# Kernel optimization log

Hardware: AMD Instinct MI355X
Metric: run time of the kernel (lower is better)

The kernel has to match this reference:

```python
import jax, jax.numpy as jnp
import numpy as np

BN_EPS = 1e-5

def _square_distance(a, b):
    # a: (B,N,3), b: (B,M,3) -> (B,N,M) squared euclidean distance
    a2 = jnp.sum(a * a, axis=-1)[:, :, None]
    b2 = jnp.sum(b * b, axis=-1)[:, None, :]
    return a2 + b2 - 2.0 * jnp.einsum('bnd,bmd->bnm', a, b)

def _bn(x, gamma, beta, mean, var):
    # eval-mode batchnorm over channel (last) dim
    return (x - mean) * jax.lax.rsqrt(var + BN_EPS) * gamma + beta

def setup_inputs() -> dict:
    key = jax.random.key(0)
    ks = jax.random.split(key, 16)
    B, M, N, D, C = 4, 2048, 16384, 64, 64
    din, dout = C + D, 64
    return {
        'xyz_down': jax.random.normal(ks[0], (B, M, 3), jnp.float32),
        'xyz_up': jax.random.normal(ks[1], (B, N, 3), jnp.float32),
        'feat_down': jax.random.normal(ks[2], (B, M, D), jnp.float32),
        'feat_up': jax.random.normal(ks[3], (B, N, C), jnp.float32),
        'W1': jax.random.normal(ks[4], (din, din), jnp.float32) * 0.05,
        'b1': jax.random.normal(ks[5], (din,), jnp.float32) * 0.05,
        'bn1_gamma': jax.random.uniform(ks[6], (din,), jnp.float32, 0.5, 1.5),
        'bn1_beta': jax.random.normal(ks[7], (din,), jnp.float32) * 0.05,
        'bn1_mean': jax.random.normal(ks[8], (din,), jnp.float32) * 0.05,
        'bn1_var': jax.random.uniform(ks[9], (din,), jnp.float32, 0.5, 1.5),
        'W2': jax.random.normal(ks[10], (dout, din), jnp.float32) * 0.05,
        'b2': jax.random.normal(ks[11], (dout,), jnp.float32) * 0.05,
        'bn2_gamma': jax.random.uniform(ks[12], (dout,), jnp.float32, 0.5, 1.5),
        'bn2_beta': jax.random.normal(ks[13], (dout,), jnp.float32) * 0.05,
        'bn2_mean': jax.random.normal(ks[14], (dout,), jnp.float32) * 0.05,
        'bn2_var': jax.random.uniform(ks[15], (dout,), jnp.float32, 0.5, 1.5),
    }

def reference(xyz_down, xyz_up, feat_down, feat_up,
              W1, b1, bn1_gamma, bn1_beta, bn1_mean, bn1_var,
              W2, b2, bn2_gamma, bn2_beta, bn2_mean, bn2_var):
    dist = _square_distance(xyz_up, xyz_down)              # (B,N,M)
    dist_recip = 1.0 / (dist + 1e-8)
    weight = dist_recip / jnp.sum(dist_recip, axis=2, keepdims=True)
    # bmm-equivalent of the original broadcast-multiply-sum
    feat_interp = jnp.einsum('bnm,bmd->bnd', weight, feat_down)  # (B,N,D)
    x = jnp.concatenate([feat_up, feat_interp], axis=-1)   # (B,N,C+D)
    # Conv1d(k=1) == pointwise linear over channel dim
    x = jnp.einsum('bnc,oc->bno', x, W1) + b1
    x = jax.nn.relu(_bn(x, bn1_gamma, bn1_beta, bn1_mean, bn1_var))
    x = jnp.einsum('bnc,oc->bno', x, W2) + b2
    x = _bn(x, bn2_gamma, bn2_beta, bn2_mean, bn2_var)
    return x
```

## Files before the change

kernel.cpp:

```cpp
#include <hip/hip_runtime.h>

typedef unsigned short u16;
typedef unsigned int   u32;
typedef unsigned long long u64;

typedef __attribute__((ext_vector_type(8))) short bf16x8;
typedef __attribute__((ext_vector_type(4))) float f32x4;

#define BB 4
#define MM 2048
#define NN 16384
#define DD 64

__device__ __forceinline__ u16 f2bf(float f) {
    union { float f; u32 u; } v; v.f = f;
    u32 r = v.u + 0x7fffu + ((v.u >> 16) & 1u);
    return (u16)(r >> 16);
}

__device__ __forceinline__ u32 pack_trunc(float hi, float lo) {
    union { float f; u32 u; } a, b; a.f = hi; b.f = lo;
    return __builtin_amdgcn_perm(a.u, b.u, 0x07060302);
}

__device__ __forceinline__ u32 pack_rne(float hi, float lo) {
    return (u32)f2bf(lo) | ((u32)f2bf(hi) << 16);
}

__device__ __forceinline__ bf16x8 pack8(float4 p, float4 q) {
    bf16x8 v;
    v[0] = (short)f2bf(p.x); v[1] = (short)f2bf(p.y);
    v[2] = (short)f2bf(p.z); v[3] = (short)f2bf(p.w);
    v[4] = (short)f2bf(q.x); v[5] = (short)f2bf(q.y);
    v[6] = (short)f2bf(q.z); v[7] = (short)f2bf(q.w);
    return v;
}

#define OFF_INTERP 0ull
#define OFF_FDT    8388608ull
#define OFF_XYZ    9437184ull
#define OFF_W1     9568256ull
#define OFF_W2     9601024ull
#define OFF_BN     9617408ull
#define WS_NEED    9618944ull

__global__ __launch_bounds__(256)
void prep4_kernel(const float* __restrict__ xyz_down,
                  const float* __restrict__ feat_down,
                  const float* __restrict__ W1, const float* __restrict__ b1,
                  const float* __restrict__ g1, const float* __restrict__ be1,
                  const float* __restrict__ m1, const float* __restrict__ v1,
                  const float* __restrict__ W2, const float* __restrict__ b2,
                  const float* __restrict__ g2, const float* __restrict__ be2,
                  const float* __restrict__ m2, const float* __restrict__ v2,
                  u16* __restrict__ fdT, float4* __restrict__ xyzd2,
                  u16* __restrict__ w1bf, u16* __restrict__ w2bf,
                  float* __restrict__ bnbuf)
{
    const int blk = blockIdx.x, t = threadIdx.x;
    if (blk < 128) {
        __shared__ u16 T[64 * 70];
        const int b = blk >> 5, m0 = (blk & 31) * 64;
        {
            const int row = t >> 2, fcb = (t & 3) * 16;
            const float4* src = (const float4*)(feat_down + ((size_t)(b * MM + m0 + row)) * 64 + fcb);
#pragma unroll
            for (int i = 0; i < 4; i++) {
                float4 v = src[i];
                union { u16 h[4]; u64 q; } pk;
                pk.h[0] = f2bf(v.x); pk.h[1] = f2bf(v.y);
                pk.h[2] = f2bf(v.z); pk.h[3] = f2bf(v.w);
                *(u64*)&T[row * 70 + fcb + i * 4] = pk.q;
            }
        }
        __syncthreads();
        {
            const int d = t & 63, w = t >> 6;
            union { u16 h[16]; uint4 q[2]; } o;
#pragma unroll
            for (int j = 0; j < 16; j++) o.h[j] = T[(w * 16 + j) * 70 + d];
            uint4* dst = (uint4*)&fdT[((size_t)(b * 64 + d)) * MM + m0 + w * 16];
            dst[0] = o.q[0];
            dst[1] = o.q[1];
        }
    } else if (blk < 160) {
        int idx = (blk - 128) * 256 + t;
        float x = xyz_down[idx * 3 + 0], y = xyz_down[idx * 3 + 1], z = xyz_down[idx * 3 + 2];
        xyzd2[idx] = make_float4(-2.f * x, -2.f * y, -2.f * z,
                                 x * x + y * y + z * z + 1e-8f);
    } else if (blk < 168) {
        int g = (blk - 160) * 256 + t;
        const float4* s = (const float4*)(W1 + g * 8);
        bf16x8 v = pack8(s[0], s[1]);
        *(bf16x8*)&w1bf[g * 8] = v;
    } else if (blk < 172) {
        int g = (blk - 168) * 256 + t;
        const float4* s = (const float4*)(W2 + g * 8);
        bf16x8 v = pack8(s[0], s[1]);
        *(bf16x8*)&w2bf[g * 8] = v;
    } else {
        if (t < 128) {
            float a = g1[t] * rsqrtf(v1[t] + 1e-5f);
            bnbuf[t] = a;
            bnbuf[128 + t] = (b1[t] - m1[t]) * a + be1[t];
        } else if (t < 192) {
            int o = t - 128;
            float a = g2[o] * rsqrtf(v2[o] + 1e-5f);
            bnbuf[256 + o] = a;
            bnbuf[320 + o] = (b2[o] - m2[o]) * a + be2[o];
        }
    }
}

__global__ __launch_bounds__(256, 4)
void interp4_kernel(const float* __restrict__ xyz_up,
                    const u16* __restrict__ fdT,
                    const float4* __restrict__ xyzd2,
                    u16* __restrict__ interp_out)
{
    __shared__ u16    ftbuf[2][64 * 72];
    __shared__ float4 xyzb[2][72];

    const int tid = threadIdx.x;
    const int b  = blockIdx.x >> 8;
    const int n0 = (blockIdx.x & 255) * 64;
    const int wave = tid >> 6;
    const int lane = tid & 63;
    const int q    = lane >> 4;
    const int nl   = lane & 15;

    const int row = n0 + wave * 16 + nl;
    const float* xu = xyz_up + ((size_t)(b * NN + row)) * 3;
    const float ax = xu[0], ay = xu[1], az = xu[2];
    const float a2 = ax * ax + ay * ay + az * az;

    f32x4 acc[4];
#pragma unroll
    for (int i = 0; i < 4; i++) acc[i] = (f32x4){0.f, 0.f, 0.f, 0.f};
    f32x4 accd = (f32x4){0.f, 0.f, 0.f, 0.f};

    bf16x8 ones;
#pragma unroll
    for (int i = 0; i < 8; i++) ones[i] = (short)0x3F80;

    const int sd = tid >> 2, sms = (tid & 3) * 16;
    const u16* fsrc = fdT + ((size_t)(b * 64 + sd)) * MM + sms;
    const float4* xsrc = xyzd2 + b * MM;

    {
        u16* fd = &ftbuf[0][sd * 72 + sms];
        *(uint4*)fd       = *(const uint4*)(fsrc);
        *(uint4*)(fd + 8) = *(const uint4*)(fsrc + 8);
        if (tid < 64) xyzb[0][tid + (tid >> 3)] = xsrc[tid];
    }
    __syncthreads();

    for (int c = 0; c < 32; ++c) {
        const int cur = c & 1, nxt = cur ^ 1;
        const bool have_next = (c + 1) < 32;
        uint4 nf0, nf1; float4 nx;
        if (have_next) {
            const int mc = (c + 1) * 64;
            nf0 = *(const uint4*)(fsrc + mc);
            nf1 = *(const uint4*)(fsrc + mc + 8);
            if (tid < 64) nx = xsrc[mc + tid];
        }

#pragma unroll
        for (int kk = 0; kk < 2; kk++) {
            u32 fr[4];
#pragma unroll
            for (int jp = 0; jp < 4; jp++) {
                int m0 = kk * 32 + q * 8 + jp * 2;
                int s0 = m0 + (m0 >> 3);
                float4 p0 = xyzb[cur][s0];
                float4 p1 = xyzb[cur][s0 + 1];
                float d0 = fmaf(p0.x, ax, fmaf(p0.y, ay, fmaf(p0.z, az, p0.w + a2)));
                float d1 = fmaf(p1.x, ax, fmaf(p1.y, ay, fmaf(p1.z, az, p1.w + a2)));
                d0 = fmaxf(d0, 1e-8f);
                d1 = fmaxf(d1, 1e-8f);
                float r0 = __builtin_amdgcn_rcpf(d0);
                float r1 = __builtin_amdgcn_rcpf(d1);
                fr[jp] = pack_trunc(r1, r0);
            }
            union { u32 u[4]; bf16x8 v; } af;
            af.u[0] = fr[0]; af.u[1] = fr[1]; af.u[2] = fr[2]; af.u[3] = fr[3];
#pragma unroll
            for (int dt = 0; dt < 4; dt++) {
                bf16x8 bb = *(bf16x8*)&ftbuf[cur][(dt * 16 + nl) * 72 + kk * 32 + q * 8];
                acc[dt] = __builtin_amdgcn_mfma_f32_16x16x32_bf16(af.v, bb, acc[dt], 0, 0, 0);
            }
            accd = __builtin_amdgcn_mfma_f32_16x16x32_bf16(af.v, ones, accd, 0, 0, 0);
        }

        if (have_next) {
            u16* fd = &ftbuf[nxt][sd * 72 + sms];
            *(uint4*)fd       = nf0;
            *(uint4*)(fd + 8) = nf1;
            if (tid < 64) xyzb[nxt][tid + (tid >> 3)] = nx;
        }
        __syncthreads();
    }

#pragma unroll
    for (int reg = 0; reg < 4; reg++) {
        int r = wave * 16 + q * 4 + reg;
        float inv = 1.0f / accd[reg];
        size_t gbase = ((size_t)(b * NN + n0 + r)) * 64;
#pragma unroll
        for (int dt = 0; dt < 4; dt++)
            interp_out[gbase + dt * 16 + nl] = f2bf(acc[dt][reg] * inv);
    }
}

__global__ __launch_bounds__(256, 2)
void mlp4_kernel(const float* __restrict__ feat_up,
                 const u16* __restrict__ interp,
                 const u16* __restrict__ w1bf,
                 const u16* __restrict__ w2bf,
                 const float* __restrict__ bnbuf,
                 float* __restrict__ out)
{
    __shared__ u16   w1L[128 * 136];
    __shared__ u16   w2L[64 * 136];
    __shared__ u16   xh[64 * 136];
    __shared__ float bnl[384];

    const int tid = threadIdx.x;
    const int b    = blockIdx.x >> 7;
    const int base = (blockIdx.x & 127) * 128;
    const int wave = tid >> 6;
    const int lane = tid & 63;
    const int q    = lane >> 4;
    const int nl   = lane & 15;

    bnl[tid] = bnbuf[tid];
    if (tid < 128) bnl[256 + tid] = bnbuf[256 + tid];

    {
        const int o = tid >> 1, h = (tid & 1) * 64;
        const uint4* src = (const uint4*)(w1bf + (size_t)o * 128 + h);
        uint4* dst = (uint4*)&w1L[o * 136 + h];
#pragma unroll
        for (int i = 0; i < 8; i++) dst[i] = src[i];
    }
    {
        const int o = tid >> 2, h = (tid & 3) * 32;
        const uint4* src = (const uint4*)(w2bf + (size_t)o * 128 + h);
        uint4* dst = (uint4*)&w2L[o * 136 + h];
#pragma unroll
        for (int i = 0; i < 4; i++) dst[i] = src[i];
    }

    for (int tile = 0; tile < 2; tile++) {
        const int n0 = base + tile * 64;
        __syncthreads();

        {
            const int r = tid >> 2, seg = (tid & 3) * 16;
            const float4* fs = (const float4*)(feat_up + ((size_t)(b * NN + n0 + r)) * 64 + seg);
            uint4* xd = (uint4*)&xh[r * 136 + seg];
            float4 f0 = fs[0], f1 = fs[1], f2 = fs[2], f3 = fs[3];
            uint4 o0, o1;
            o0.x = pack_rne(f0.y, f0.x); o0.y = pack_rne(f0.w, f0.z);
            o0.z = pack_rne(f1.y, f1.x); o0.w = pack_rne(f1.w, f1.z);
            o1.x = pack_rne(f2.y, f2.x); o1.y = pack_rne(f2.w, f2.z);
            o1.z = pack_rne(f3.y, f3.x); o1.w = pack_rne(f3.w, f3.z);
            xd[0] = o0; xd[1] = o1;
            const uint4* is = (const uint4*)(interp + ((size_t)(b * NN + n0 + r)) * 64 + seg);
            uint4* xd2 = (uint4*)&xh[r * 136 + 64 + seg];
            xd2[0] = is[0]; xd2[1] = is[1];
        }
        __syncthreads();

        f32x4 acc1[8];
#pragma unroll
        for (int i = 0; i < 8; i++) acc1[i] = (f32x4){0.f, 0.f, 0.f, 0.f};
#pragma unroll
        for (int k0 = 0; k0 < 128; k0 += 32) {
            bf16x8 af = *(bf16x8*)&xh[(wave * 16 + nl) * 136 + k0 + q * 8];
#pragma unroll
            for (int ot = 0; ot < 8; ot++) {
                bf16x8 bf = *(bf16x8*)&w1L[(ot * 16 + nl) * 136 + k0 + q * 8];
                acc1[ot] = __builtin_amdgcn_mfma_f32_16x16x32_bf16(af, bf, acc1[ot], 0, 0, 0);
            }
        }
        __syncthreads();

#pragma unroll
        for (int ot = 0; ot < 8; ot++) {
            int o = ot * 16 + nl;
            float aa = bnl[o], bc = bnl[128 + o];
#pragma unroll
            for (int reg = 0; reg < 4; reg++) {
                float v = fmaxf(fmaf(acc1[ot][reg], aa, bc), 0.f);
                xh[(wave * 16 + q * 4 + reg) * 136 + o] = f2bf(v);
            }
        }
        __syncthreads();

        f32x4 acc2[4];
#pragma unroll
        for (int i = 0; i < 4; i++) acc2[i] = (f32x4){0.f, 0.f, 0.f, 0.f};
#pragma unroll
        for (int k0 = 0; k0 < 128; k0 += 32) {
            bf16x8 af = *(bf16x8*)&xh[(wave * 16 + nl) * 136 + k0 + q * 8];
#pragma unroll
            for (int ot = 0; ot < 4; ot++) {
                bf16x8 bf = *(bf16x8*)&w2L[(ot * 16 + nl) * 136 + k0 + q * 8];
                acc2[ot] = __builtin_amdgcn_mfma_f32_16x16x32_bf16(af, bf, acc2[ot], 0, 0, 0);
            }
        }
        float* of = (float*)xh;
#pragma unroll
        for (int ot = 0; ot < 4; ot++) {
            int o = ot * 16 + nl;
            float aa = bnl[256 + o], bc = bnl[320 + o];
#pragma unroll
            for (int reg = 0; reg < 4; reg++)
                of[(wave * 16 + q * 4 + reg) * 68 + o] = fmaf(acc2[ot][reg], aa, bc);
        }
        __syncthreads();

        {
            const int r = tid >> 2, seg = (tid & 3) * 16;
            const float4* sf = (const float4*)&of[r * 68 + seg];
            float4* dst = (float4*)(out + ((size_t)(b * NN + n0 + r)) * 64 + seg);
#pragma unroll
            for (int i = 0; i < 4; i++) dst[i] = sf[i];
        }
    }
}

#define TN 128
#define BM 64
#define RS 72
#define FS 72

__global__ __launch_bounds__(256, 3)
void interp_kernel(const float* __restrict__ xyz_down,
                   const float* __restrict__ xyz_up,
                   const float* __restrict__ feat_down,
                   u16* __restrict__ interp_out)
{
    __shared__ u16   rbuf[TN * RS];
    __shared__ u16   ftbuf[DD * FS];
    __shared__ float xyzb[BM * 3];
    __shared__ float denp[TN * 2];
    __shared__ float invden[TN];

    const int tid = threadIdx.x;
    const int b  = blockIdx.x >> 7;
    const int n0 = (blockIdx.x & 127) * TN;

    const int nl_r = tid >> 1;
    const int half = tid & 1;
    const float* xu = xyz_up + (size_t)(b * NN + n0 + nl_r) * 3;
    const float ax = xu[0], ay = xu[1], az = xu[2];

    denp[tid] = 0.f;

    const int wave = tid >> 6;
    const int lane = tid & 63;
    const int q    = lane >> 4;
    const int nl   = lane & 15;

    f32x4 acc[2][4];
#pragma unroll
    for (int i = 0; i < 2; i++)
#pragma unroll
        for (int j = 0; j < 4; j++) acc[i][j] = (f32x4){0.f, 0.f, 0.f, 0.f};

    const int sm = (tid & 31) * 2;
    const int sd = (tid >> 5) * 8;

    for (int mc = 0; mc < MM; mc += BM) {
        __syncthreads();
        if (tid < 192) xyzb[tid] = xyz_down[(size_t)(b * MM + mc) * 3 + tid];
        {
            const float4* f0 = (const float4*)(feat_down + (size_t)(b * MM + mc + sm) * DD + sd);
            const float4* f1 = (const float4*)(feat_down + (size_t)(b * MM + mc + sm + 1) * DD + sd);
            float4 a0 = f0[0], a1 = f0[1];
            float4 b0 = f1[0], b1 = f1[1];
            float r0[8] = {a0.x, a0.y, a0.z, a0.w, a1.x, a1.y, a1.z, a1.w};
            float r1[8] = {b0.x, b0.y, b0.z, b0.w, b1.x, b1.y, b1.z, b1.w};
#pragma unroll
            for (int j = 0; j < 8; j++) {
                u32 pk = (u32)f2bf(r0[j]) | ((u32)f2bf(r1[j]) << 16);
                *(u32*)&ftbuf[(sd + j) * FS + sm] = pk;
            }
        }
        __syncthreads();
        {
            float dlc = 0.f;
#pragma unroll
            for (int s = 0; s < 4; s++) {
                bf16x8 v;
#pragma unroll
                for (int j = 0; j < 8; j++) {
                    int m = half * 32 + s * 8 + j;
                    float dx = ax - xyzb[3 * m + 0];
                    float dy = ay - xyzb[3 * m + 1];
                    float dz = az - xyzb[3 * m + 2];
                    float d = fmaf(dx, dx, fmaf(dy, dy, dz * dz)) + 1e-8f;
                    float r = __builtin_amdgcn_rcpf(d);
                    dlc += r;
                    v[j] = (short)f2bf(r);
                }
                *(bf16x8*)&rbuf[nl_r * RS + half * 32 + s * 8] = v;
            }
            denp[nl_r * 2 + half] += dlc;
        }
        __syncthreads();
        {
            const int rowbase = wave * 32;
#pragma unroll
            for (int k0 = 0; k0 < BM; k0 += 32) {
                bf16x8 a0 = *(bf16x8*)&rbuf[(rowbase + nl) * RS + k0 + q * 8];
                bf16x8 a1 = *(bf16x8*)&rbuf[(rowbase + 16 + nl) * RS + k0 + q * 8];
#pragma unroll
                for (int dt = 0; dt < 4; dt++) {
                    bf16x8 bb = *(bf16x8*)&ftbuf[(dt * 16 + nl) * FS + k0 + q * 8];
                    acc[0][dt] = __builtin_amdgcn_mfma_f32_16x16x32_bf16(a0, bb, acc[0][dt], 0, 0, 0);
                    acc[1][dt] = __builtin_amdgcn_mfma_f32_16x16x32_bf16(a1, bb, acc[1][dt], 0, 0, 0);
                }
            }
        }
    }

    __syncthreads();
    if (tid < TN) invden[tid] = 1.0f / (denp[tid * 2] + denp[tid * 2 + 1]);
    __syncthreads();
    {
        const int rowbase = wave * 32;
#pragma unroll
        for (int nt = 0; nt < 2; nt++) {
#pragma unroll
            for (int reg = 0; reg < 4; reg++) {
                int nloc = rowbase + nt * 16 + q * 4 + reg;
                float inv = invden[nloc];
                size_t gbase = (size_t)(b * NN + n0 + nloc) * DD;
#pragma unroll
                for (int dt = 0; dt < 4; dt++)
                    interp_out[gbase + dt * 16 + nl] = f2bf(acc[nt][dt][reg] * inv);
            }
        }
    }
}

#define T2 64

__global__ __launch_bounds__(256, 1)
void mlp_kernel(const float* __restrict__ feat_up,
                const u16*   __restrict__ interp,
                const float* __restrict__ W1, const float* __restrict__ b1,
                const float* __restrict__ g1, const float* __restrict__ be1,
                const float* __restrict__ m1, const float* __restrict__ v1,
                const float* __restrict__ W2, const float* __restrict__ b2,
                const float* __restrict__ g2, const float* __restrict__ be2,
                const float* __restrict__ m2, const float* __restrict__ v2,
                float* __restrict__ out)
{
    __shared__ u16 xb[T2 * 136];
    __shared__ u16 hb[T2 * 136];
    __shared__ u16 w1b[128 * 136];
    __shared__ u16 w2b[64 * 136];
    __shared__ float A1[128], Bc1[128], A2[64], Bc2[64];

    const int tid = threadIdx.x;
    const int b  = blockIdx.x >> 8;
    const int n0 = (blockIdx.x & 255) * T2;
    const int wave = tid >> 6;
    const int lane = tid & 63;
    const int q    = lane >> 4;
    const int nl   = lane & 15;

    if (tid < 128) {
        float a = g1[tid] * rsqrtf(v1[tid] + 1e-5f);
        A1[tid]  = a;
        Bc1[tid] = (b1[tid] - m1[tid]) * a + be1[tid];
    } else if (tid < 192) {
        int o = tid - 128;
        float a = g2[o] * rsqrtf(v2[o] + 1e-5f);
        A2[o]  = a;
        Bc2[o] = (b2[o] - m2[o]) * a + be2[o];
    }
    {
        const float4* src = (const float4*)(W1 + (size_t)(tid >> 1) * 128 + (tid & 1) * 64);
        u16* dst = &w1b[(tid >> 1) * 136 + (tid & 1) * 64];
#pragma unroll
        for (int i = 0; i < 8; i++)
            *(bf16x8*)(dst + 8 * i) = pack8(src[2 * i], src[2 * i + 1]);
    }
    {
        const float4* src = (const float4*)(W2 + (size_t)(tid >> 2) * 128 + (tid & 3) * 32);
        u16* dst = &w2b[(tid >> 2) * 136 + (tid & 3) * 32];
#pragma unroll
        for (int i = 0; i < 4; i++)
            *(bf16x8*)(dst + 8 * i) = pack8(src[2 * i], src[2 * i + 1]);
    }
    if (tid < 128) {
        int n = tid >> 1, hf = tid & 1;
        const float4* src = (const float4*)(feat_up + (size_t)(b * NN + n0 + n) * 64 + hf * 32);
        u16* dst = &xb[n * 136 + hf * 32];
#pragma unroll
        for (int i = 0; i < 4; i++)
            *(bf16x8*)(dst + 8 * i) = pack8(src[2 * i], src[2 * i + 1]);
    } else {
        int t2 = tid - 128;
        int n = t2 >> 1, hf = t2 & 1;
        const uint4* src = (const uint4*)(interp + (size_t)(b * NN + n0 + n) * 64 + hf * 32);
        u16* dst = &xb[n * 136 + 64 + hf * 32];
#pragma unroll
        for (int i = 0; i < 4; i++)
            *(uint4*)(dst + 8 * i) = src[i];
    }
    __syncthreads();

    f32x4 acc1[8];
#pragma unroll
    for (int i = 0; i < 8; i++) acc1[i] = (f32x4){0.f, 0.f, 0.f, 0.f};
#pragma unroll
    for (int k0 = 0; k0 < 128; k0 += 32) {
        bf16x8 a = *(bf16x8*)&xb[(wave * 16 + nl) * 136 + k0 + q * 8];
#pragma unroll
        for (int ot = 0; ot < 8; ot++) {
            bf16x8 bb = *(bf16x8*)&w1b[(ot * 16 + nl) * 136 + k0 + q * 8];
            acc1[ot] = __builtin_amdgcn_mfma_f32_16x16x32_bf16(a, bb, acc1[ot], 0, 0, 0);
        }
    }
#pragma unroll
    for (int ot = 0; ot < 8; ot++) {
        int o = ot * 16 + nl;
        float aa = A1[o], bc = Bc1[o];
#pragma unroll
        for (int reg = 0; reg < 4; reg++) {
            float v = fmaxf(fmaf(acc1[ot][reg], aa, bc), 0.f);
            hb[(wave * 16 + q * 4 + reg) * 136 + o] = f2bf(v);
        }
    }
    __syncthreads();

    f32x4 acc2[4];
#pragma unroll
    for (int i = 0; i < 4; i++) acc2[i] = (f32x4){0.f, 0.f, 0.f, 0.f};
#pragma unroll
    for (int k0 = 0; k0 < 128; k0 += 32) {
        bf16x8 a = *(bf16x8*)&hb[(wave * 16 + nl) * 136 + k0 + q * 8];
#pragma unroll
        for (int ot = 0; ot < 4; ot++) {
            bf16x8 bb = *(bf16x8*)&w2b[(ot * 16 + nl) * 136 + k0 + q * 8];
            acc2[ot] = __builtin_amdgcn_mfma_f32_16x16x32_bf16(a, bb, acc2[ot], 0, 0, 0);
        }
    }
#pragma unroll
    for (int ot = 0; ot < 4; ot++) {
        int o = ot * 16 + nl;
        float aa = A2[o], bc = Bc2[o];
#pragma unroll
        for (int reg = 0; reg < 4; reg++)
            out[(size_t)(b * NN + n0 + wave * 16 + q * 4 + reg) * 64 + o] =
                fmaf(acc2[ot][reg], aa, bc);
    }
}

extern "C" void kernel_launch(void* const* d_in, const int* in_sizes, int n_in,
                              void* d_out, int out_size, void* d_ws, size_t ws_size,
                              hipStream_t stream) {
    const float* xyz_down  = (const float*)d_in[0];
    const float* xyz_up    = (const float*)d_in[1];
    const float* feat_down = (const float*)d_in[2];
    const float* feat_up   = (const float*)d_in[3];
    const float* W1  = (const float*)d_in[4];
    const float* b1  = (const float*)d_in[5];
    const float* g1  = (const float*)d_in[6];
    const float* be1 = (const float*)d_in[7];
    const float* m1  = (const float*)d_in[8];
    const float* v1  = (const float*)d_in[9];
    const float* W2  = (const float*)d_in[10];
    const float* b2  = (const float*)d_in[11];
    const float* g2  = (const float*)d_in[12];
    const float* be2 = (const float*)d_in[13];
    const float* m2  = (const float*)d_in[14];
    const float* v2  = (const float*)d_in[15];
    float* out = (float*)d_out;
    char* ws = (char*)d_ws;

    if (ws_size >= WS_NEED) {
        u16*    interp = (u16*)(ws + OFF_INTERP);
        u16*    fdT    = (u16*)(ws + OFF_FDT);
        float4* xyzd2  = (float4*)(ws + OFF_XYZ);
        u16*    w1bf   = (u16*)(ws + OFF_W1);
        u16*    w2bf   = (u16*)(ws + OFF_W2);
        float*  bnbuf  = (float*)(ws + OFF_BN);

        prep4_kernel<<<dim3(173), dim3(256), 0, stream>>>(
            xyz_down, feat_down, W1, b1, g1, be1, m1, v1,
            W2, b2, g2, be2, m2, v2, fdT, xyzd2, w1bf, w2bf, bnbuf);
        interp4_kernel<<<dim3(BB * (NN / 64)), dim3(256), 0, stream>>>(
            xyz_up, fdT, xyzd2, interp);
        mlp4_kernel<<<dim3(BB * (NN / 128)), dim3(256), 0, stream>>>(
            feat_up, interp, w1bf, w2bf, bnbuf, out);
    } else {
        u16* interp = (u16*)d_ws;
        interp_kernel<<<dim3(BB * (NN / TN)), dim3(256), 0, stream>>>(
            xyz_down, xyz_up, feat_down, interp);
        mlp_kernel<<<dim3(BB * (NN / T2)), dim3(256), 0, stream>>>(
            feat_up, interp, W1, b1, g1, be1, m1, v1,
            W2, b2, g2, be2, m2, v2, out);
    }
}
```

Measured before the change: 156.9 us.

## Fuse interpolation and MLP into one kernel with pre-swizzled weights

Result: slower. 181.0 us (+15.4%).

```diff
diff --git a/kernel.cpp b/kernel.cpp
--- a/kernel.cpp
+++ b/kernel.cpp
@@ -6,6 +6,7 @@
 
 typedef __attribute__((ext_vector_type(8))) short bf16x8;
 typedef __attribute__((ext_vector_type(4))) float f32x4;
+typedef __attribute__((ext_vector_type(2))) float f32x2;
 
 #define BB 4
 #define MM 2048
@@ -36,16 +37,15 @@
     return v;
 }
 
-#define OFF_INTERP 0ull
-#define OFF_FDT    8388608ull
-#define OFF_XYZ    9437184ull
-#define OFF_W1     9568256ull
-#define OFF_W2     9601024ull
-#define OFF_BN     9617408ull
-#define WS_NEED    9618944ull
+#define OFF_FDT   0ull
+#define OFF_XYZP  1048576ull
+#define OFF_W1S   1179648ull
+#define OFF_W2S   1212416ull
+#define OFF_BN    1228800ull
+#define WS_NEED   1230336ull
 
 __global__ __launch_bounds__(256)
-void prep4_kernel(const float* __restrict__ xyz_down,
+void prep5_kernel(const float* __restrict__ xyz_down,
                   const float* __restrict__ feat_down,
                   const float* __restrict__ W1, const float* __restrict__ b1,
                   const float* __restrict__ g1, const float* __restrict__ be1,
@@ -53,8 +53,8 @@
                   const float* __restrict__ W2, const float* __restrict__ b2,
                   const float* __restrict__ g2, const float* __restrict__ be2,
                   const float* __restrict__ m2, const float* __restrict__ v2,
-                  u16* __restrict__ fdT, float4* __restrict__ xyzd2,
-                  u16* __restrict__ w1bf, u16* __restrict__ w2bf,
+                  u16* __restrict__ fdT, float4* __restrict__ xyzP,
+                  u16* __restrict__ w1s, u16* __restrict__ w2s,
                   float* __restrict__ bnbuf)
 {
     const int blk = blockIdx.x, t = threadIdx.x;
@@ -83,21 +83,32 @@
             dst[0] = o.q[0];
             dst[1] = o.q[1];
         }
-    } else if (blk < 160) {
-        int idx = (blk - 128) * 256 + t;
-        float x = xyz_down[idx * 3 + 0], y = xyz_down[idx * 3 + 1], z = xyz_down[idx * 3 + 2];
-        xyzd2[idx] = make_float4(-2.f * x, -2.f * y, -2.f * z,
-                                 x * x + y * y + z * z + 1e-8f);
-    } else if (blk < 168) {
-        int g = (blk - 160) * 256 + t;
-        const float4* s = (const float4*)(W1 + g * 8);
-        bf16x8 v = pack8(s[0], s[1]);
-        *(bf16x8*)&w1bf[g * 8] = v;
-    } else if (blk < 172) {
-        int g = (blk - 168) * 256 + t;
-        const float4* s = (const float4*)(W2 + g * 8);
-        bf16x8 v = pack8(s[0], s[1]);
-        *(bf16x8*)&w2bf[g * 8] = v;
+    } else if (blk < 144) {
+        int g = (blk - 128) * 256 + t;
+        int b = g >> 10, p = g & 1023;
+        const float* s = xyz_down + ((size_t)b * MM + 2 * p) * 3;
+        float x0 = s[0], y0 = s[1], z0 = s[2];
+        float x1 = s[3], y1 = s[4], z1 = s[5];
+        float w0 = x0 * x0 + y0 * y0 + z0 * z0 + 1e-8f;
+        float w1v = x1 * x1 + y1 * y1 + z1 * z1 + 1e-8f;
+        xyzP[(size_t)g * 2 + 0] = make_float4(-2.f * x0, -2.f * x1, -2.f * y0, -2.f * y1);
+        xyzP[(size_t)g * 2 + 1] = make_float4(-2.f * z0, -2.f * z1, w0, w1v);
+    } else if (blk < 152) {
+        int slot = (blk - 144) * 256 + t;
+        int f = slot >> 6, l = slot & 63;
+        int kg = f >> 3, ot = f & 7;
+        int o = ot * 16 + (l & 15), c = kg * 32 + (l >> 4) * 8;
+        const float4* src = (const float4*)(W1 + (size_t)o * 128 + c);
+        bf16x8 v = pack8(src[0], src[1]);
+        *(bf16x8*)&w1s[(size_t)slot * 8] = v;
+    } else if (blk < 156) {
+        int slot = (blk - 152) * 256 + t;
+        int f = slot >> 6, l = slot & 63;
+        int kg = f >> 2, ot = f & 3;
+        int o = ot * 16 + (l & 15), c = kg * 32 + (l >> 4) * 8;
+        const float4* src = (const float4*)(W2 + (size_t)o * 128 + c);
+        bf16x8 v = pack8(src[0], src[1]);
+        *(bf16x8*)&w2s[(size_t)slot * 8] = v;
     } else {
         if (t < 128) {
             float a = g1[t] * rsqrtf(v1[t] + 1e-5f);
@@ -113,13 +124,18 @@
 }
 
 __global__ __launch_bounds__(256, 4)
-void interp4_kernel(const float* __restrict__ xyz_up,
-                    const u16* __restrict__ fdT,
-                    const float4* __restrict__ xyzd2,
-                    u16* __restrict__ interp_out)
+void fused6_kernel(const float* __restrict__ xyz_up,
+                   const u16* __restrict__ fdT,
+                   const float4* __restrict__ xyzP,
+                   const float* __restrict__ feat_up,
+                   const u16* __restrict__ w1s,
+                   const u16* __restrict__ w2s,
+                   const float* __restrict__ bnbuf,
+                   float* __restrict__ out)
 {
-    __shared__ u16    ftbuf[2][64 * 72];
-    __shared__ float4 xyzb[2][72];
+    __shared__ u16   ftbuf[2][64 * 72];
+    __shared__ u16   xh[64 * 136];
+    __shared__ float bnl[384];
 
     const int tid = threadIdx.x;
     const int b  = blockIdx.x >> 8;
@@ -129,10 +145,29 @@
     const int q    = lane >> 4;
     const int nl   = lane & 15;
 
+    bnl[tid] = bnbuf[tid];
+    if (tid < 128) bnl[256 + tid] = bnbuf[256 + tid];
+
+    {
+        const int r = tid >> 2, seg = (tid & 3) * 16;
+        const float4* fs = (const float4*)(feat_up + ((size_t)(b * NN + n0 + r)) * 64 + seg);
+        float4 f0 = fs[0], f1 = fs[1], f2 = fs[2], f3 = fs[3];
+        uint4 o0, o1;
+        o0.x = pack_rne(f0.y, f0.x); o0.y = pack_rne(f0.w, f0.z);
+        o0.z = pack_rne(f1.y, f1.x); o0.w = pack_rne(f1.w, f1.z);
+        o1.x = pack_rne(f2.y, f2.x); o1.y = pack_rne(f2.w, f2.z);
+        o1.z = pack_rne(f3.y, f3.x); o1.w = pack_rne(f3.w, f3.z);
+        uint4* xd = (uint4*)&xh[r * 136 + seg];
+        xd[0] = o0; xd[1] = o1;
+    }
+
     const int row = n0 + wave * 16 + nl;
     const float* xu = xyz_up + ((size_t)(b * NN + row)) * 3;
     const float ax = xu[0], ay = xu[1], az = xu[2];
-    const float a2 = ax * ax + ay * ay + az * az;
+    const f32x2 ax2 = (f32x2){ax, ax}, ay2 = (f32x2){ay, ay}, az2 = (f32x2){az, az};
+    const f32x2 a22 = (f32x2){ax * ax + ay * ay + az * az,
+                              ax * ax + ay * ay + az * az};
+    const f32x2 eps2 = (f32x2){1e-8f, 1e-8f};
 
     f32x4 acc[4];
 #pragma unroll
@@ -145,25 +180,23 @@
 
     const int sd = tid >> 2, sms = (tid & 3) * 16;
     const u16* fsrc = fdT + ((size_t)(b * 64 + sd)) * MM + sms;
-    const float4* xsrc = xyzd2 + b * MM;
+    const float4* xb = xyzP + (size_t)b * 2048;
 
     {
         u16* fd = &ftbuf[0][sd * 72 + sms];
         *(uint4*)fd       = *(const uint4*)(fsrc);
         *(uint4*)(fd + 8) = *(const uint4*)(fsrc + 8);
-        if (tid < 64) xyzb[0][tid + (tid >> 3)] = xsrc[tid];
     }
     __syncthreads();
 
     for (int c = 0; c < 32; ++c) {
         const int cur = c & 1, nxt = cur ^ 1;
         const bool have_next = (c + 1) < 32;
-        uint4 nf0, nf1; float4 nx;
+        uint4 nf0, nf1;
         if (have_next) {
             const int mc = (c + 1) * 64;
             nf0 = *(const uint4*)(fsrc + mc);
             nf1 = *(const uint4*)(fsrc + mc + 8);
-            if (tid < 64) nx = xsrc[mc + tid];
         }
 
 #pragma unroll
@@ -171,16 +204,19 @@
             u32 fr[4];
 #pragma unroll
             for (int jp = 0; jp < 4; jp++) {
-                int m0 = kk * 32 + q * 8 + jp * 2;
-                int s0 = m0 + (m0 >> 3);
-                float4 p0 = xyzb[cur][s0];
-                float4 p1 = xyzb[cur][s0 + 1];
-                float d0 = fmaf(p0.x, ax, fmaf(p0.y, ay, fmaf(p0.z, az, p0.w + a2)));
-                float d1 = fmaf(p1.x, ax, fmaf(p1.y, ay, fmaf(p1.z, az, p1.w + a2)));
-                d0 = fmaxf(d0, 1e-8f);
-                d1 = fmaxf(d1, 1e-8f);
-                float r0 = __builtin_amdgcn_rcpf(d0);
-                float r1 = __builtin_amdgcn_rcpf(d1);
+                const float4* pp = xb + (size_t)(c * 32 + kk * 16 + q * 4 + jp) * 2;
+                float4 ld0 = pp[0];
+                float4 ld1 = pp[1];
+                f32x2 px = (f32x2){ld0.x, ld0.y};
+                f32x2 py = (f32x2){ld0.z, ld0.w};
+                f32x2 pz = (f32x2){ld1.x, ld1.y};
+                f32x2 pw = (f32x2){ld1.z, ld1.w};
+                f32x2 d = __builtin_elementwise_fma(px, ax2,
+                          __builtin_elementwise_fma(py, ay2,
+                          __builtin_elementwise_fma(pz, az2, pw + a22)));
+                d = __builtin_elementwise_max(d, eps2);
+                float r0 = __builtin_amdgcn_rcpf(d.x);
+                float r1 = __builtin_amdgcn_rcpf(d.y);
                 fr[jp] = pack_trunc(r1, r0);
             }
             union { u32 u[4]; bf16x8 v; } af;
@@ -197,138 +233,73 @@
             u16* fd = &ftbuf[nxt][sd * 72 + sms];
             *(uint4*)fd       = nf0;
             *(uint4*)(fd + 8) = nf1;
-            if (tid < 64) xyzb[nxt][tid + (tid >> 3)] = nx;
         }
         __syncthreads();
     }
 
 #pragma unroll
     for (int reg = 0; reg < 4; reg++) {
-        int r = wave * 16 + q * 4 + reg;
         float inv = 1.0f / accd[reg];
-        size_t gbase = ((size_t)(b * NN + n0 + r)) * 64;
+        int rl = wave * 16 + q * 4 + reg;
 #pragma unroll
         for (int dt = 0; dt < 4; dt++)
-            interp_out[gbase + dt * 16 + nl] = f2bf(acc[dt][reg] * inv);
-    }
-}
-
-__global__ __launch_bounds__(256, 2)
-void mlp4_kernel(const float* __restrict__ feat_up,
-                 const u16* __restrict__ interp,
-                 const u16* __restrict__ w1bf,
-                 const u16* __restrict__ w2bf,
-                 const float* __restrict__ bnbuf,
-                 float* __restrict__ out)
-{
-    __shared__ u16   w1L[128 * 136];
-    __shared__ u16   w2L[64 * 136];
-    __shared__ u16   xh[64 * 136];
-    __shared__ float bnl[384];
-
-    const int tid = threadIdx.x;
-    const int b    = blockIdx.x >> 7;
-    const int base = (blockIdx.x & 127) * 128;
-    const int wave = tid >> 6;
-    const int lane = tid & 63;
-    const int q    = lane >> 4;
-    const int nl   = lane & 15;
-
-    bnl[tid] = bnbuf[tid];
-    if (tid < 128) bnl[256 + tid] = bnbuf[256 + tid];
+            xh[rl * 136 + 64 + dt * 16 + nl] = f2bf(acc[dt][reg] * inv);
+    }
+    __syncthreads();
+
+    f32x4 acc1[8];
+#pragma unroll
+    for (int i = 0; i < 8; i++) acc1[i] = (f32x4){0.f, 0.f, 0.f, 0.f};
+#pragma unroll
+    for (int kg = 0; kg < 4; kg++) {
+        bf16x8 af = *(bf16x8*)&xh[(wave * 16 + nl) * 136 + kg * 32 + q * 8];
+#pragma unroll
+        for (int ot = 0; ot < 8; ot++) {
+            bf16x8 bf = *(const bf16x8*)(w1s + ((size_t)(kg * 8 + ot) * 64 + lane) * 8);
+            acc1[ot] = __builtin_amdgcn_mfma_f32_16x16x32_bf16(af, bf, acc1[ot], 0, 0, 0);
+        }
+    }
+#pragma unroll
+    for (int ot = 0; ot < 8; ot++) {
+        int o = ot * 16 + nl;
+        float aa = bnl[o], bc = bnl[128 + o];
+#pragma unroll
+        for (int reg = 0; reg < 4; reg++) {
+            float v = fmaxf(fmaf(acc1[ot][reg], aa, bc), 0.f);
+            xh[(wave * 16 + q * 4 + reg) * 136 + o] = f2bf(v);
+        }
+    }
+    __syncthreads();
+
+    f32x4 acc2[4];
+#pragma unroll
+    for (int i = 0; i < 4; i++) acc2[i] = (f32x4){0.f, 0.f, 0.f, 0.f};
+#pragma unroll
+    for (int kg = 0; kg < 4; kg++) {
+        bf16x8 af = *(bf16x8*)&xh[(wave * 16 + nl) * 136 + kg * 32 + q * 8];
+#pragma unroll
+        for (int ot = 0; ot < 4; ot++) {
+            bf16x8 bf = *(const bf16x8*)(w2s + ((size_t)(kg * 4 + ot) * 64 + lane) * 8);
+            acc2[ot] = __builtin_amdgcn_mfma_f32_16x16x32_bf16(af, bf, acc2[ot], 0, 0, 0);
+        }
+    }
+    float* of = (float*)xh;
+#pragma unroll
+    for (int ot = 0; ot < 4; ot++) {
+        int o = ot * 16 + nl;
+        float aa = bnl[256 + o], bc = bnl[320 + o];
+#pragma unroll
+        for (int reg = 0; reg < 4; reg++)
+            of[(wave * 16 + q * 4 + reg) * 68 + o] = fmaf(acc2[ot][reg], aa, bc);
+    }
+    __syncthreads();
 
     {
-        const int o = tid >> 1, h = (tid & 1) * 64;
-        const uint4* src = (const uint4*)(w1bf + (size_t)o * 128 + h);
-        uint4* dst = (uint4*)&w1L[o * 136 + h];
-#pragma unroll
-        for (int i = 0; i < 8; i++) dst[i] = src[i];
-    }
-    {
-        const int o = tid >> 2, h = (tid & 3) * 32;
-        const uint4* src = (const uint4*)(w2bf + (size_t)o * 128 + h);
-        uint4* dst = (uint4*)&w2L[o * 136 + h];
-#pragma unroll
-        for (int i = 0; i < 4; i++) dst[i] = src[i];
-    }
-
-    for (int tile = 0; tile < 2; tile++) {
-        const int n0 = base + tile * 64;
-        __syncthreads();
-
-        {
-            const int r = tid >> 2, seg = (tid & 3) * 16;
-            const float4* fs = (const float4*)(feat_up + ((size_t)(b * NN + n0 + r)) * 64 + seg);
-            uint4* xd = (uint4*)&xh[r * 136 + seg];
-            float4 f0 = fs[0], f1 = fs[1], f2 = fs[2], f3 = fs[3];
-            uint4 o0, o1;
-            o0.x = pack_rne(f0.y, f0.x); o0.y = pack_rne(f0.w, f0.z);
-            o0.z = pack_rne(f1.y, f1.x); o0.w = pack_rne(f1.w, f1.z);
-            o1.x = pack_rne(f2.y, f2.x); o1.y = pack_rne(f2.w, f2.z);
-            o1.z = pack_rne(f3.y, f3.x); o1.w = pack_rne(f3.w, f3.z);
-            xd[0] = o0; xd[1] = o1;
-            const uint4* is = (const uint4*)(interp + ((size_t)(b * NN + n0 + r)) * 64 + seg);
-            uint4* xd2 = (uint4*)&xh[r * 136 + 64 + seg];
-            xd2[0] = is[0]; xd2[1] = is[1];
-        }
-        __syncthreads();
-
-        f32x4 acc1[8];
-#pragma unroll
-        for (int i = 0; i < 8; i++) acc1[i] = (f32x4){0.f, 0.f, 0.f, 0.f};
-#pragma unroll
-        for (int k0 = 0; k0 < 128; k0 += 32) {
-            bf16x8 af = *(bf16x8*)&xh[(wave * 16 + nl) * 136 + k0 + q * 8];
-#pragma unroll
-            for (int ot = 0; ot < 8; ot++) {
-                bf16x8 bf = *(bf16x8*)&w1L[(ot * 16 + nl) * 136 + k0 + q * 8];
-                acc1[ot] = __builtin_amdgcn_mfma_f32_16x16x32_bf16(af, bf, acc1[ot], 0, 0, 0);
-            }
-        }
-        __syncthreads();
-
-#pragma unroll
-        for (int ot = 0; ot < 8; ot++) {
-            int o = ot * 16 + nl;
-            float aa = bnl[o], bc = bnl[128 + o];
-#pragma unroll
-            for (int reg = 0; reg < 4; reg++) {
-                float v = fmaxf(fmaf(acc1[ot][reg], aa, bc), 0.f);
-                xh[(wave * 16 + q * 4 + reg) * 136 + o] = f2bf(v);
-            }
-        }
-        __syncthreads();
-
-        f32x4 acc2[4];
-#pragma unroll
-        for (int i = 0; i < 4; i++) acc2[i] = (f32x4){0.f, 0.f, 0.f, 0.f};
-#pragma unroll
-        for (int k0 = 0; k0 < 128; k0 += 32) {
-            bf16x8 af = *(bf16x8*)&xh[(wave * 16 + nl) * 136 + k0 + q * 8];
-#pragma unroll
-            for (int ot = 0; ot < 4; ot++) {
-                bf16x8 bf = *(bf16x8*)&w2L[(ot * 16 + nl) * 136 + k0 + q * 8];
-                acc2[ot] = __builtin_amdgcn_mfma_f32_16x16x32_bf16(af, bf, acc2[ot], 0, 0, 0);
-            }
-        }
-        float* of = (float*)xh;
-#pragma unroll
-        for (int ot = 0; ot < 4; ot++) {
-            int o = ot * 16 + nl;
-            float aa = bnl[256 + o], bc = bnl[320 + o];
-#pragma unroll
-            for (int reg = 0; reg < 4; reg++)
-                of[(wave * 16 + q * 4 + reg) * 68 + o] = fmaf(acc2[ot][reg], aa, bc);
-        }
-        __syncthreads();
-
-        {
-            const int r = tid >> 2, seg = (tid & 3) * 16;
-            const float4* sf = (const float4*)&of[r * 68 + seg];
-            float4* dst = (float4*)(out + ((size_t)(b * NN + n0 + r)) * 64 + seg);
-#pragma unroll
-            for (int i = 0; i < 4; i++) dst[i] = sf[i];
-        }
+        const int r = tid >> 2, seg = (tid & 3) * 16;
+        const float4* sf = (const float4*)&of[r * 68 + seg];
+        float4* dst = (float4*)(out + ((size_t)(b * NN + n0 + r)) * 64 + seg);
+#pragma unroll
+        for (int i = 0; i < 4; i++) dst[i] = sf[i];
     }
 }
 
@@ -587,20 +558,17 @@
     char* ws = (char*)d_ws;
 
     if (ws_size >= WS_NEED) {
-        u16*    interp = (u16*)(ws + OFF_INTERP);
-        u16*    fdT    = (u16*)(ws + OFF_FDT);
-        float4* xyzd2  = (float4*)(ws + OFF_XYZ);
-        u16*    w1bf   = (u16*)(ws + OFF_W1);
-        u16*    w2bf   = (u16*)(ws + OFF_W2);
-        float*  bnbuf  = (float*)(ws + OFF_BN);
-
-        prep4_kernel<<<dim3(173), dim3(256), 0, stream>>>(
+        u16*    fdT   = (u16*)(ws + OFF_FDT);
+        float4* xyzP  = (float4*)(ws + OFF_XYZP);
+        u16*    w1s   = (u16*)(ws + OFF_W1S);
+        u16*    w2s   = (u16*)(ws + OFF_W2S);
+        float*  bnbuf = (float*)(ws + OFF_BN);
+
+        prep5_kernel<<<dim3(157), dim3(256), 0, stream>>>(
             xyz_down, feat_down, W1, b1, g1, be1, m1, v1,
-            W2, b2, g2, be2, m2, v2, fdT, xyzd2, w1bf, w2bf, bnbuf);
-        interp4_kernel<<<dim3(BB * (NN / 64)), dim3(256), 0, stream>>>(
-            xyz_up, fdT, xyzd2, interp);
-        mlp4_kernel<<<dim3(BB * (NN / 128)), dim3(256), 0, stream>>>(
-            feat_up, interp, w1bf, w2bf, bnbuf, out);
+            W2, b2, g2, be2, m2, v2, fdT, xyzP, w1s, w2s, bnbuf);
+        fused6_kernel<<<dim3(BB * (NN / 64)), dim3(256), 0, stream>>>(
+            xyz_up, fdT, xyzP, feat_up, w1s, w2s, bnbuf, out);
     } else {
         u16* interp = (u16*)d_ws;
         interp_kernel<<<dim3(BB * (NN / TN)), dim3(256), 0, stream>>>(
```
